# Performance work log

Hardware: AMD Instinct MI355X
Metric: run time of the kernel (lower is better)

The kernel has to match this reference:

```python
import jax, jax.numpy as jnp
import numpy as np

N = 100000   # nodes
E = 1600000  # edges (before self-loops)
H1, C1 = 8, 16   # conv1: heads=8, out_channels=16
H2, C2 = 1, 1    # conv2: heads=1, out_channels=1
NEG_SLOPE = 0.2
EPS = 1e-16


def setup_inputs() -> dict:
    key = jax.random.key(0)
    ks = jax.random.split(key, 10)
    s = 0.3
    return {
        "x": jax.random.normal(ks[0], (N, 1), jnp.float32),
        "edge_index": jax.random.randint(ks[1], (2, E), 0, N, dtype=jnp.int64),
        "W1": jax.random.normal(ks[2], (1, H1 * C1), jnp.float32) * s,
        "att_src1": jax.random.normal(ks[3], (1, H1, C1), jnp.float32) * s,
        "att_dst1": jax.random.normal(ks[4], (1, H1, C1), jnp.float32) * s,
        "b1": jax.random.normal(ks[5], (H1 * C1,), jnp.float32) * s,
        "W2": jax.random.normal(ks[6], (H1 * C1, H2 * C2), jnp.float32) * s,
        "att_src2": jax.random.normal(ks[7], (1, H2, C2), jnp.float32) * s,
        "att_dst2": jax.random.normal(ks[8], (1, H2, C2), jnp.float32) * s,
        "b2": jax.random.normal(ks[9], (C2,), jnp.float32) * s,
    }


def gat_conv(x, src, dst, W, att_src, att_dst, bias, heads, ch, concat):
    # Linear projection, split into heads: [N, H, C]
    h = (x @ W).reshape(-1, heads, ch)
    # Per-node attention logits: [N, H]
    a_src = (h * att_src).sum(-1)
    a_dst = (h * att_dst).sum(-1)
    # Edge-wise score with LeakyReLU: [E, H]
    e = jax.nn.leaky_relu(a_src[src] + a_dst[dst], NEG_SLOPE)
    # Segment softmax over incoming edges of each dst node
    m = jax.ops.segment_max(e, dst, num_segments=N)
    ex = jnp.exp(e - m[dst])
    denom = jax.ops.segment_sum(ex, dst, num_segments=N)
    alpha = ex / (denom[dst] + EPS)                      # [E, H]
    # Weighted scatter-add aggregation: [N, H, C]
    out = jax.ops.segment_sum(h[src] * alpha[:, :, None], dst, num_segments=N)
    out = out.reshape(-1, heads * ch) if concat else out.mean(axis=1)
    return out + bias


def reference(x, edge_index, W1, att_src1, att_dst1, b1, W2, att_src2, att_dst2, b2):
    # PyG GATConv default add_self_loops=True
    loop = jnp.arange(N, dtype=edge_index.dtype)
    src = jnp.concatenate([edge_index[0], loop])
    dst = jnp.concatenate([edge_index[1], loop])
    # dropout p=0.6 is identity in eval mode
    h = gat_conv(x, src, dst, W1, att_src1, att_dst1, b1, H1, C1, concat=True)
    h = jax.nn.elu(h)
    out = gat_conv(h, src, dst, W2, att_src2, att_dst2, b2, H2, C2, concat=False)
    return out  # [N, 1]
```

## Files before the change

kernel.cpp:

```cpp
#include <hip/hip_runtime.h>

#define NEG_SLOPE 0.2f
#define EPSV 1e-16f
#define NHEADS 8
#define NCH 16
#define BKT_SHIFT 8
#define BKT_NODES 256
#define CAP 8192
#define BIN_EPB 4096
#define MAX_BKT 512

__global__ __launch_bounds__(512) void gat_setup_kernel(
        const float* __restrict__ W1, const float* __restrict__ as1,
        const float* __restrict__ ad1, float* __restrict__ S1,
        float* __restrict__ D1, int* __restrict__ bkt_cnt, int nbuckets) {
    int t = threadIdx.x;
    for (int i = t; i < nbuckets; i += 512) bkt_cnt[i] = 0;
    if (t < NHEADS) {
        float s = 0.f, d = 0.f;
        for (int c = 0; c < NCH; ++c) {
            float w = W1[t * NCH + c];
            s += w * as1[t * NCH + c];
            d += w * ad1[t * NCH + c];
        }
        S1[t] = s;
        D1[t] = d;
    }
}

__global__ __launch_bounds__(256) void gat_bin_kernel(
        const int* __restrict__ ei, int E, int nbuckets,
        int* __restrict__ bkt_cnt, unsigned int* __restrict__ binned) {
    __shared__ int hist[MAX_BKT];
    __shared__ int gbase[MAX_BKT];
    int t = threadIdx.x;
    for (int i = t; i < nbuckets; i += 256) hist[i] = 0;
    __syncthreads();
    int base = blockIdx.x * BIN_EPB;
    int lr[BIN_EPB / 256];
#pragma unroll
    for (int k = 0; k < BIN_EPB / 1024; ++k) {
        int idx = base + k * 1024 + t * 4;
        if (idx + 3 < E) {
            int4 d4 = *(const int4*)(ei + E + idx);
            lr[4 * k + 0] = atomicAdd(&hist[d4.x >> BKT_SHIFT], 1);
            lr[4 * k + 1] = atomicAdd(&hist[d4.y >> BKT_SHIFT], 1);
            lr[4 * k + 2] = atomicAdd(&hist[d4.z >> BKT_SHIFT], 1);
            lr[4 * k + 3] = atomicAdd(&hist[d4.w >> BKT_SHIFT], 1);
        } else {
            for (int u = 0; u < 4; ++u)
                if (idx + u < E)
                    lr[4 * k + u] = atomicAdd(&hist[ei[E + idx + u] >> BKT_SHIFT], 1);
        }
    }
    __syncthreads();
    for (int i = t; i < nbuckets; i += 256) {
        int c = hist[i];
        gbase[i] = c ? (i * CAP + atomicAdd(&bkt_cnt[i], c)) : 0;
    }
    __syncthreads();
#pragma unroll
    for (int k = 0; k < BIN_EPB / 1024; ++k) {
        int idx = base + k * 1024 + t * 4;
        if (idx + 3 < E) {
            int4 s4 = *(const int4*)(ei + idx);
            int4 d4 = *(const int4*)(ei + E + idx);
            binned[gbase[d4.x >> BKT_SHIFT] + lr[4 * k + 0]] =
                ((unsigned int)s4.x << BKT_SHIFT) | (unsigned int)(d4.x & (BKT_NODES - 1));
            binned[gbase[d4.y >> BKT_SHIFT] + lr[4 * k + 1]] =
                ((unsigned int)s4.y << BKT_SHIFT) | (unsigned int)(d4.y & (BKT_NODES - 1));
            binned[gbase[d4.z >> BKT_SHIFT] + lr[4 * k + 2]] =
                ((unsigned int)s4.z << BKT_SHIFT) | (unsigned int)(d4.z & (BKT_NODES - 1));
            binned[gbase[d4.w >> BKT_SHIFT] + lr[4 * k + 3]] =
                ((unsigned int)s4.w << BKT_SHIFT) | (unsigned int)(d4.w & (BKT_NODES - 1));
        } else {
            for (int u = 0; u < 4; ++u)
                if (idx + u < E) {
                    unsigned int s = (unsigned int)ei[idx + u];
                    int d = ei[E + idx + u];
                    binned[gbase[d >> BKT_SHIFT] + lr[4 * k + u]] =
                        (s << BKT_SHIFT) | (unsigned int)(d & (BKT_NODES - 1));
                }
        }
    }
}

__global__ __launch_bounds__(256) void gat_gather1_kernel(
        int N, const float* __restrict__ x,
        unsigned int* __restrict__ binned, const int* __restrict__ bkt_cnt,
        const float* __restrict__ S1g, const float* __restrict__ D1g,
        const float* __restrict__ W1, const float* __restrict__ b1,
        const float* __restrict__ W2, float* __restrict__ h2out,
        int* __restrict__ row_start, int* __restrict__ row_deg) {
    __shared__ unsigned int ed[CAP];
    __shared__ int cnt[BKT_NODES];
    __shared__ int off[BKT_NODES];
    __shared__ int cur[BKT_NODES];
    __shared__ float xloc[BKT_NODES];
    int b = blockIdx.x, t = threadIdx.x;
    int node = (b << BKT_SHIFT) + t;
    xloc[t] = (node < N) ? x[node] : 0.f;
    cnt[t] = 0;
    __syncthreads();
    int nE = bkt_cnt[b]; if (nE > CAP) nE = CAP;
    const unsigned int* bb = binned + (size_t)b * CAP;
    for (int j0 = 0; j0 < nE; j0 += 1024) {
        int idx = j0 + t * 4;
        if (idx + 3 < nE) {
            uint4 q = *(const uint4*)(bb + idx);
            atomicAdd(&cnt[q.x & (BKT_NODES - 1)], 1);
            atomicAdd(&cnt[q.y & (BKT_NODES - 1)], 1);
            atomicAdd(&cnt[q.z & (BKT_NODES - 1)], 1);
            atomicAdd(&cnt[q.w & (BKT_NODES - 1)], 1);
        } else {
            for (int u = 0; u < 4; ++u)
                if (idx + u < nE) atomicAdd(&cnt[bb[idx + u] & (BKT_NODES - 1)], 1);
        }
    }
    __syncthreads();
    int c = cnt[t];
    off[t] = c;
    __syncthreads();
    for (int o = 1; o < 256; o <<= 1) {
        int v = (t >= o) ? off[t - o] : 0;
        __syncthreads();
        off[t] += v;
        __syncthreads();
    }
    int o_excl = off[t] - c;
    off[t] = o_excl;
    cur[t] = o_excl;
    __syncthreads();
    for (int j0 = 0; j0 < nE; j0 += 1024) {
        int idx = j0 + t * 4;
        if (idx + 3 < nE) {
            uint4 q = *(const uint4*)(bb + idx);
            ed[atomicAdd(&cur[q.x & (BKT_NODES - 1)], 1)] = q.x >> BKT_SHIFT;
            ed[atomicAdd(&cur[q.y & (BKT_NODES - 1)], 1)] = q.y >> BKT_SHIFT;
            ed[atomicAdd(&cur[q.z & (BKT_NODES - 1)], 1)] = q.z >> BKT_SHIFT;
            ed[atomicAdd(&cur[q.w & (BKT_NODES - 1)], 1)] = q.w >> BKT_SHIFT;
        } else {
            for (int u = 0; u < 4; ++u)
                if (idx + u < nE) {
                    unsigned int v = bb[idx + u];
                    ed[atomicAdd(&cur[v & (BKT_NODES - 1)], 1)] = v >> BKT_SHIFT;
                }
        }
    }
    __syncthreads();
    for (int j0 = 0; j0 < nE; j0 += 1024) {
        int idx = j0 + t * 4;
        if (idx + 3 < nE) {
            *(uint4*)(binned + (size_t)b * CAP + idx) = *(const uint4*)(ed + idx);
        } else {
            for (int u = 0; u < 4; ++u)
                if (idx + u < nE) binned[(size_t)b * CAP + idx + u] = ed[idx + u];
        }
    }
    if (node < N) {
        row_start[node] = b * CAP + o_excl;
        row_deg[node] = c;
    }
    float S1[NHEADS], A[NHEADS], den[NHEADS], num[NHEADS];
    float xn = xloc[t];
#pragma unroll
    for (int h = 0; h < NHEADS; ++h) {
        S1[h] = S1g[h];
        A[h] = xn * D1g[h];
        float e = xn * S1[h] + A[h];
        e = e > 0.f ? e : NEG_SLOPE * e;
        float ex = __expf(e);
        den[h] = ex + EPSV;
        num[h] = ex * xn;
    }
    int j = 0;
    for (; j + 4 <= c; j += 4) {
        unsigned int e0 = ed[o_excl + j + 0], e1 = ed[o_excl + j + 1];
        unsigned int e2 = ed[o_excl + j + 2], e3 = ed[o_excl + j + 3];
        float x0 = x[e0], x1 = x[e1], x2 = x[e2], x3 = x[e3];
#pragma unroll
        for (int h = 0; h < NHEADS; ++h) {
            float ea = x0 * S1[h] + A[h]; ea = ea > 0.f ? ea : NEG_SLOPE * ea;
            float eb = x1 * S1[h] + A[h]; eb = eb > 0.f ? eb : NEG_SLOPE * eb;
            float ec = x2 * S1[h] + A[h]; ec = ec > 0.f ? ec : NEG_SLOPE * ec;
            float ee = x3 * S1[h] + A[h]; ee = ee > 0.f ? ee : NEG_SLOPE * ee;
            float fa = __expf(ea), fb = __expf(eb), fc = __expf(ec), fd = __expf(ee);
            den[h] += (fa + fb) + (fc + fd);
            num[h] += (fa * x0 + fb * x1) + (fc * x2 + fd * x3);
        }
    }
    for (; j < c; ++j) {
        unsigned int e0 = ed[o_excl + j];
        float x0 = x[e0];
#pragma unroll
        for (int h = 0; h < NHEADS; ++h) {
            float ea = x0 * S1[h] + A[h];
            ea = ea > 0.f ? ea : NEG_SLOPE * ea;
            float fa = __expf(ea);
            den[h] += fa;
            num[h] += fa * x0;
        }
    }
    if (node >= N) return;
    float acc = 0.f;
#pragma unroll
    for (int h = 0; h < NHEADS; ++h) {
        float z = num[h] / den[h];
#pragma unroll
        for (int cc = 0; cc < NCH; ++cc) {
            int k = h * NCH + cc;
            float vv = W1[k] * z + b1[k];
            vv = vv > 0.f ? vv : (__expf(vv) - 1.f);
            acc += vv * W2[k];
        }
    }
    h2out[node] = acc;
}

__global__ __launch_bounds__(256) void gat_gather2_kernel(
        int N, const float* __restrict__ h2,
        const unsigned int* __restrict__ binned,
        const int* __restrict__ row_start, const int* __restrict__ row_deg,
        const float* __restrict__ as2p, const float* __restrict__ ad2p,
        const float* __restrict__ b2, float* __restrict__ out) {
    int n = blockIdx.x * blockDim.x + threadIdx.x;
    if (n >= N) return;
    float a_s = as2p[0], a_d = ad2p[0];
    float hn = h2[n];
    float ad = hn * a_d;
    float e = hn * a_s + ad;
    e = e > 0.f ? e : NEG_SLOPE * e;
    float ex = __expf(e);
    float den = ex + EPSV;
    float num = ex * hn;
    int st = row_start[n], dg = row_deg[n];
    int j = 0;
    for (; j + 4 <= dg; j += 4) {
        unsigned int e0 = binned[st + j + 0], e1 = binned[st + j + 1];
        unsigned int e2 = binned[st + j + 2], e3 = binned[st + j + 3];
        float h0 = h2[e0], h1 = h2[e1], h3 = h2[e2], h4 = h2[e3];
        float ea = h0 * a_s + ad; ea = ea > 0.f ? ea : NEG_SLOPE * ea;
        float eb = h1 * a_s + ad; eb = eb > 0.f ? eb : NEG_SLOPE * eb;
        float ec = h3 * a_s + ad; ec = ec > 0.f ? ec : NEG_SLOPE * ec;
        float ee = h4 * a_s + ad; ee = ee > 0.f ? ee : NEG_SLOPE * ee;
        float fa = __expf(ea), fb = __expf(eb), fc = __expf(ec), fd = __expf(ee);
        den += (fa + fb) + (fc + fd);
        num += (fa * h0 + fb * h1) + (fc * h3 + fd * h4);
    }
    for (; j < dg; ++j) {
        unsigned int e0 = binned[st + j];
        float h0 = h2[e0];
        float ea = h0 * a_s + ad;
        ea = ea > 0.f ? ea : NEG_SLOPE * ea;
        float fa = __expf(ea);
        den += fa;
        num += fa * h0;
    }
    out[n] = num / den + b2[0];
}

extern "C" void kernel_launch(void* const* d_in, const int* in_sizes, int n_in,
                              void* d_out, int out_size, void* d_ws, size_t ws_size,
                              hipStream_t stream) {
    const float* x   = (const float*)d_in[0];
    const int*   ei  = (const int*)d_in[1];
    const float* W1  = (const float*)d_in[2];
    const float* as1 = (const float*)d_in[3];
    const float* ad1 = (const float*)d_in[4];
    const float* b1  = (const float*)d_in[5];
    const float* W2  = (const float*)d_in[6];
    const float* as2 = (const float*)d_in[7];
    const float* ad2 = (const float*)d_in[8];
    const float* b2  = (const float*)d_in[9];
    float* out = (float*)d_out;

    int N = in_sizes[0];
    int E = in_sizes[1] / 2;

    int nbuckets = (N + BKT_NODES - 1) >> BKT_SHIFT;
    int nbin     = (E + BIN_EPB - 1) / BIN_EPB;
    int nb       = (N + 255) / 256;

    float* S1        = (float*)d_ws;
    float* D1        = S1 + 8;
    float* h2        = D1 + 8;
    int*   row_start = (int*)(h2 + N);
    int*   row_deg   = row_start + N;
    int*   bkt_cnt   = row_deg + N;
    unsigned int* binned = (unsigned int*)(bkt_cnt + nbuckets);

    gat_setup_kernel<<<1, 512, 0, stream>>>(W1, as1, ad1, S1, D1,
                                            bkt_cnt, nbuckets);
    gat_bin_kernel<<<nbin, 256, 0, stream>>>(ei, E, nbuckets, bkt_cnt, binned);
    gat_gather1_kernel<<<nbuckets, 256, 0, stream>>>(N, x, binned, bkt_cnt,
                                                     S1, D1, W1, b1, W2, h2,
                                                     row_start, row_deg);
    gat_gather2_kernel<<<nb, 256, 0, stream>>>(N, h2, binned, row_start, row_deg,
                                               as2, ad2, b2, out);
}
```

Baseline: 135.5 us.

## Fuse binning and both GAT layers into one cooperative kernel with grid syncs

Merges the setup, binning, layer-1 gather and layer-2 gather kernels into a single cooperative launch that uses grid-wide syncs between phases. The per-bucket sorted edge list stays in shared memory through layer 2, so the sorted list, row_start and row_deg are no longer written back to global memory. Layer 2 reuses each node's own h2 from a register. The cost is two grid barriers, a grid of about 391 blocks that must all be co-resident (launch bounds of 256 threads, 2 per CU), and an extra memset call.

```diff
diff --git a/kernel.cpp b/kernel.cpp
--- a/kernel.cpp
+++ b/kernel.cpp
@@ -1,4 +1,7 @@
 #include <hip/hip_runtime.h>
+#include <hip/hip_cooperative_groups.h>
+
+namespace cg = cooperative_groups;
 
 #define NEG_SLOPE 0.2f
 #define EPSV 1e-16f
@@ -10,12 +13,25 @@
 #define BIN_EPB 4096
 #define MAX_BKT 512
 
-__global__ __launch_bounds__(512) void gat_setup_kernel(
+__global__ __launch_bounds__(256, 2) void gat_fused_kernel(
+        int N, int E, int nbuckets,
+        const float* __restrict__ x, const int* __restrict__ ei,
         const float* __restrict__ W1, const float* __restrict__ as1,
-        const float* __restrict__ ad1, float* __restrict__ S1,
-        float* __restrict__ D1, int* __restrict__ bkt_cnt, int nbuckets) {
-    int t = threadIdx.x;
-    for (int i = t; i < nbuckets; i += 512) bkt_cnt[i] = 0;
+        const float* __restrict__ ad1, const float* __restrict__ b1,
+        const float* __restrict__ W2, const float* __restrict__ as2,
+        const float* __restrict__ ad2, const float* __restrict__ b2,
+        int* __restrict__ bkt_cnt, unsigned int* __restrict__ binned,
+        float* __restrict__ h2, float* __restrict__ out) {
+    cg::grid_group grid = cg::this_grid();
+    __shared__ unsigned int ed[CAP];
+    __shared__ int cnt[BKT_NODES];
+    __shared__ int cur[BKT_NODES];
+    __shared__ int offs[BKT_NODES];
+    __shared__ float xloc[BKT_NODES];
+    __shared__ float sS1[NHEADS], sD1[NHEADS];
+
+    int b = blockIdx.x, t = threadIdx.x;
+
     if (t < NHEADS) {
         float s = 0.f, d = 0.f;
         for (int c = 0; c < NCH; ++c) {
@@ -23,20 +39,14 @@
             s += w * as1[t * NCH + c];
             d += w * ad1[t * NCH + c];
         }
-        S1[t] = s;
-        D1[t] = d;
-    }
-}
-
-__global__ __launch_bounds__(256) void gat_bin_kernel(
-        const int* __restrict__ ei, int E, int nbuckets,
-        int* __restrict__ bkt_cnt, unsigned int* __restrict__ binned) {
-    __shared__ int hist[MAX_BKT];
-    __shared__ int gbase[MAX_BKT];
-    int t = threadIdx.x;
+        sS1[t] = s; sD1[t] = d;
+    }
+
+    int* hist  = (int*)&ed[0];
+    int* gbase = hist + MAX_BKT;
     for (int i = t; i < nbuckets; i += 256) hist[i] = 0;
     __syncthreads();
-    int base = blockIdx.x * BIN_EPB;
+    int base = b * BIN_EPB;
     int lr[BIN_EPB / 256];
 #pragma unroll
     for (int k = 0; k < BIN_EPB / 1024; ++k) {
@@ -83,26 +93,16 @@
                 }
         }
     }
-}
-
-__global__ __launch_bounds__(256) void gat_gather1_kernel(
-        int N, const float* __restrict__ x,
-        unsigned int* __restrict__ binned, const int* __restrict__ bkt_cnt,
-        const float* __restrict__ S1g, const float* __restrict__ D1g,
-        const float* __restrict__ W1, const float* __restrict__ b1,
-        const float* __restrict__ W2, float* __restrict__ h2out,
-        int* __restrict__ row_start, int* __restrict__ row_deg) {
-    __shared__ unsigned int ed[CAP];
-    __shared__ int cnt[BKT_NODES];
-    __shared__ int off[BKT_NODES];
-    __shared__ int cur[BKT_NODES];
-    __shared__ float xloc[BKT_NODES];
-    int b = blockIdx.x, t = threadIdx.x;
+    __threadfence();
+    grid.sync();
+
     int node = (b << BKT_SHIFT) + t;
-    xloc[t] = (node < N) ? x[node] : 0.f;
+    float xn = (node < N) ? x[node] : 0.f;
+    xloc[t] = xn;
     cnt[t] = 0;
     __syncthreads();
-    int nE = bkt_cnt[b]; if (nE > CAP) nE = CAP;
+    int nE = (b < nbuckets) ? bkt_cnt[b] : 0;
+    if (nE > CAP) nE = CAP;
     const unsigned int* bb = binned + (size_t)b * CAP;
     for (int j0 = 0; j0 < nE; j0 += 1024) {
         int idx = j0 + t * 4;
@@ -119,16 +119,15 @@
     }
     __syncthreads();
     int c = cnt[t];
-    off[t] = c;
+    offs[t] = c;
     __syncthreads();
     for (int o = 1; o < 256; o <<= 1) {
-        int v = (t >= o) ? off[t - o] : 0;
+        int v = (t >= o) ? offs[t - o] : 0;
         __syncthreads();
-        off[t] += v;
+        offs[t] += v;
         __syncthreads();
     }
-    int o_excl = off[t] - c;
-    off[t] = o_excl;
+    int o_excl = offs[t] - c;
     cur[t] = o_excl;
     __syncthreads();
     for (int j0 = 0; j0 < nE; j0 += 1024) {
@@ -148,25 +147,11 @@
         }
     }
     __syncthreads();
-    for (int j0 = 0; j0 < nE; j0 += 1024) {
-        int idx = j0 + t * 4;
-        if (idx + 3 < nE) {
-            *(uint4*)(binned + (size_t)b * CAP + idx) = *(const uint4*)(ed + idx);
-        } else {
-            for (int u = 0; u < 4; ++u)
-                if (idx + u < nE) binned[(size_t)b * CAP + idx + u] = ed[idx + u];
-        }
-    }
-    if (node < N) {
-        row_start[node] = b * CAP + o_excl;
-        row_deg[node] = c;
-    }
     float S1[NHEADS], A[NHEADS], den[NHEADS], num[NHEADS];
-    float xn = xloc[t];
 #pragma unroll
     for (int h = 0; h < NHEADS; ++h) {
-        S1[h] = S1g[h];
-        A[h] = xn * D1g[h];
+        S1[h] = sS1[h];
+        A[h] = xn * sD1[h];
         float e = xn * S1[h] + A[h];
         e = e > 0.f ? e : NEG_SLOPE * e;
         float ex = __expf(e);
@@ -201,62 +186,53 @@
             num[h] += fa * x0;
         }
     }
-    if (node >= N) return;
-    float acc = 0.f;
+    float h2val = 0.f;
 #pragma unroll
     for (int h = 0; h < NHEADS; ++h) {
         float z = num[h] / den[h];
 #pragma unroll
-        for (int cc = 0; cc < NCH; ++cc) {
-            int k = h * NCH + cc;
+        for (int ccc = 0; ccc < NCH; ++ccc) {
+            int k = h * NCH + ccc;
             float vv = W1[k] * z + b1[k];
             vv = vv > 0.f ? vv : (__expf(vv) - 1.f);
-            acc += vv * W2[k];
-        }
-    }
-    h2out[node] = acc;
-}
-
-__global__ __launch_bounds__(256) void gat_gather2_kernel(
-        int N, const float* __restrict__ h2,
-        const unsigned int* __restrict__ binned,
-        const int* __restrict__ row_start, const int* __restrict__ row_deg,
-        const float* __restrict__ as2p, const float* __restrict__ ad2p,
-        const float* __restrict__ b2, float* __restrict__ out) {
-    int n = blockIdx.x * blockDim.x + threadIdx.x;
-    if (n >= N) return;
-    float a_s = as2p[0], a_d = ad2p[0];
-    float hn = h2[n];
-    float ad = hn * a_d;
-    float e = hn * a_s + ad;
-    e = e > 0.f ? e : NEG_SLOPE * e;
-    float ex = __expf(e);
-    float den = ex + EPSV;
-    float num = ex * hn;
-    int st = row_start[n], dg = row_deg[n];
-    int j = 0;
-    for (; j + 4 <= dg; j += 4) {
-        unsigned int e0 = binned[st + j + 0], e1 = binned[st + j + 1];
-        unsigned int e2 = binned[st + j + 2], e3 = binned[st + j + 3];
+            h2val += vv * W2[k];
+        }
+    }
+    if (node < N) h2[node] = h2val;
+    __threadfence();
+    grid.sync();
+
+    float a_s = as2[0], a_d = ad2[0];
+    float hn = h2val;
+    float adc = hn * a_d;
+    float e2s = hn * (a_s + a_d);
+    e2s = e2s > 0.f ? e2s : NEG_SLOPE * e2s;
+    float ex2 = __expf(e2s);
+    float den2 = ex2 + EPSV;
+    float num2 = ex2 * hn;
+    j = 0;
+    for (; j + 4 <= c; j += 4) {
+        unsigned int e0 = ed[o_excl + j + 0], e1 = ed[o_excl + j + 1];
+        unsigned int e2 = ed[o_excl + j + 2], e3 = ed[o_excl + j + 3];
         float h0 = h2[e0], h1 = h2[e1], h3 = h2[e2], h4 = h2[e3];
-        float ea = h0 * a_s + ad; ea = ea > 0.f ? ea : NEG_SLOPE * ea;
-        float eb = h1 * a_s + ad; eb = eb > 0.f ? eb : NEG_SLOPE * eb;
-        float ec = h3 * a_s + ad; ec = ec > 0.f ? ec : NEG_SLOPE * ec;
-        float ee = h4 * a_s + ad; ee = ee > 0.f ? ee : NEG_SLOPE * ee;
+        float ea = h0 * a_s + adc; ea = ea > 0.f ? ea : NEG_SLOPE * ea;
+        float eb = h1 * a_s + adc; eb = eb > 0.f ? eb : NEG_SLOPE * eb;
+        float ec = h3 * a_s + adc; ec = ec > 0.f ? ec : NEG_SLOPE * ec;
+        float ee = h4 * a_s + adc; ee = ee > 0.f ? ee : NEG_SLOPE * ee;
         float fa = __expf(ea), fb = __expf(eb), fc = __expf(ec), fd = __expf(ee);
-        den += (fa + fb) + (fc + fd);
-        num += (fa * h0 + fb * h1) + (fc * h3 + fd * h4);
-    }
-    for (; j < dg; ++j) {
-        unsigned int e0 = binned[st + j];
+        den2 += (fa + fb) + (fc + fd);
+        num2 += (fa * h0 + fb * h1) + (fc * h3 + fd * h4);
+    }
+    for (; j < c; ++j) {
+        unsigned int e0 = ed[o_excl + j];
         float h0 = h2[e0];
-        float ea = h0 * a_s + ad;
+        float ea = h0 * a_s + adc;
         ea = ea > 0.f ? ea : NEG_SLOPE * ea;
         float fa = __expf(ea);
-        den += fa;
-        num += fa * h0;
-    }
-    out[n] = num / den + b2[0];
+        den2 += fa;
+        num2 += fa * h0;
+    }
+    if (node < N) out[node] = num2 / den2 + b2[0];
 }
 
 extern "C" void kernel_launch(void* const* d_in, const int* in_sizes, int n_in,
@@ -279,22 +255,18 @@
 
     int nbuckets = (N + BKT_NODES - 1) >> BKT_SHIFT;
     int nbin     = (E + BIN_EPB - 1) / BIN_EPB;
-    int nb       = (N + 255) / 256;
-
-    float* S1        = (float*)d_ws;
-    float* D1        = S1 + 8;
-    float* h2        = D1 + 8;
-    int*   row_start = (int*)(h2 + N);
-    int*   row_deg   = row_start + N;
-    int*   bkt_cnt   = row_deg + N;
+    int nblocks  = nbuckets > nbin ? nbuckets : nbin;
+
+    float* h2      = (float*)d_ws;
+    int*   bkt_cnt = (int*)(h2 + N);
     unsigned int* binned = (unsigned int*)(bkt_cnt + nbuckets);
 
-    gat_setup_kernel<<<1, 512, 0, stream>>>(W1, as1, ad1, S1, D1,
-                                            bkt_cnt, nbuckets);
-    gat_bin_kernel<<<nbin, 256, 0, stream>>>(ei, E, nbuckets, bkt_cnt, binned);
-    gat_gather1_kernel<<<nbuckets, 256, 0, stream>>>(N, x, binned, bkt_cnt,
-                                                     S1, D1, W1, b1, W2, h2,
-                                                     row_start, row_deg);
-    gat_gather2_kernel<<<nb, 256, 0, stream>>>(N, h2, binned, row_start, row_deg,
-                                               as2, ad2, b2, out);
+    hipMemsetAsync(bkt_cnt, 0, (size_t)nbuckets * sizeof(int), stream);
+
+    void* args[] = {
+        &N, &E, &nbuckets, &x, &ei, &W1, &as1, &ad1, &b1, &W2,
+        &as2, &ad2, &b2, &bkt_cnt, &binned, &h2, &out
+    };
+    hipLaunchCooperativeKernel((void*)gat_fused_kernel, dim3(nblocks), dim3(256),
+                               args, 0, stream);
 }
```

Result: slower. 331.6 us (+144.8%).

## Shrink buckets to 64 nodes and split each node's edges across four threads

Applied to the files above, without the earlier changes.

Buckets shrink from 256 to 64 nodes, giving about 1563 gather1 blocks instead of 391, so more CUs stay busy. Within a block, four threads share each node's edge list and combine partial softmax sums through shared-memory atomics. Gather2 likewise splits each node's edges across four lanes and reduces them with shuffles. The setup kernel is removed: the per-head projections are computed inside gather1 and the bucket-count reset becomes a memset. The risks are a larger bin histogram (1600 entries of shared memory), more shared-atomic traffic, and a per-bucket capacity of 2048 edges that could truncate an unusually dense bucket.

```diff
diff --git a/kernel.cpp b/kernel.cpp
--- a/kernel.cpp
+++ b/kernel.cpp
@@ -4,35 +4,17 @@
 #define EPSV 1e-16f
 #define NHEADS 8
 #define NCH 16
-#define BKT_SHIFT 8
-#define BKT_NODES 256
-#define CAP 8192
-#define BIN_EPB 4096
-#define MAX_BKT 512
-
-__global__ __launch_bounds__(512) void gat_setup_kernel(
-        const float* __restrict__ W1, const float* __restrict__ as1,
-        const float* __restrict__ ad1, float* __restrict__ S1,
-        float* __restrict__ D1, int* __restrict__ bkt_cnt, int nbuckets) {
-    int t = threadIdx.x;
-    for (int i = t; i < nbuckets; i += 512) bkt_cnt[i] = 0;
-    if (t < NHEADS) {
-        float s = 0.f, d = 0.f;
-        for (int c = 0; c < NCH; ++c) {
-            float w = W1[t * NCH + c];
-            s += w * as1[t * NCH + c];
-            d += w * ad1[t * NCH + c];
-        }
-        S1[t] = s;
-        D1[t] = d;
-    }
-}
+#define BKT_SHIFT 6
+#define BKT_NODES 64
+#define CAP 2048
+#define BIN_EPB 8192
+#define NBKT_MAX 1600
 
 __global__ __launch_bounds__(256) void gat_bin_kernel(
         const int* __restrict__ ei, int E, int nbuckets,
         int* __restrict__ bkt_cnt, unsigned int* __restrict__ binned) {
-    __shared__ int hist[MAX_BKT];
-    __shared__ int gbase[MAX_BKT];
+    __shared__ int hist[NBKT_MAX];
+    __shared__ int gbase[NBKT_MAX];
     int t = threadIdx.x;
     for (int i = t; i < nbuckets; i += 256) hist[i] = 0;
     __syncthreads();
@@ -88,57 +70,72 @@
 __global__ __launch_bounds__(256) void gat_gather1_kernel(
         int N, const float* __restrict__ x,
         unsigned int* __restrict__ binned, const int* __restrict__ bkt_cnt,
-        const float* __restrict__ S1g, const float* __restrict__ D1g,
-        const float* __restrict__ W1, const float* __restrict__ b1,
+        const float* __restrict__ W1, const float* __restrict__ as1,
+        const float* __restrict__ ad1, const float* __restrict__ b1,
         const float* __restrict__ W2, float* __restrict__ h2out,
         int* __restrict__ row_start, int* __restrict__ row_deg) {
     __shared__ unsigned int ed[CAP];
-    __shared__ int cnt[BKT_NODES];
-    __shared__ int off[BKT_NODES];
-    __shared__ int cur[BKT_NODES];
+    __shared__ int cnt[BKT_NODES], offs[BKT_NODES], cur[BKT_NODES];
     __shared__ float xloc[BKT_NODES];
+    __shared__ float sS1[NHEADS], sD1[NHEADS];
+    __shared__ float accD[NHEADS][BKT_NODES];
+    __shared__ float accN[NHEADS][BKT_NODES];
     int b = blockIdx.x, t = threadIdx.x;
-    int node = (b << BKT_SHIFT) + t;
-    xloc[t] = (node < N) ? x[node] : 0.f;
-    cnt[t] = 0;
+    int loc = t & (BKT_NODES - 1);
+    int q = t >> BKT_SHIFT;
+    if (t < NHEADS) {
+        float s = 0.f, d = 0.f;
+        for (int c = 0; c < NCH; ++c) {
+            float w = W1[t * NCH + c];
+            s += w * as1[t * NCH + c];
+            d += w * ad1[t * NCH + c];
+        }
+        sS1[t] = s; sD1[t] = d;
+    }
+    if (t < BKT_NODES) {
+        int node = (b << BKT_SHIFT) + t;
+        xloc[t] = (node < N) ? x[node] : 0.f;
+        cnt[t] = 0;
+    }
+    for (int i = t; i < NHEADS * BKT_NODES; i += 256) {
+        (&accD[0][0])[i] = 0.f;
+        (&accN[0][0])[i] = 0.f;
+    }
     __syncthreads();
     int nE = bkt_cnt[b]; if (nE > CAP) nE = CAP;
     const unsigned int* bb = binned + (size_t)b * CAP;
     for (int j0 = 0; j0 < nE; j0 += 1024) {
         int idx = j0 + t * 4;
         if (idx + 3 < nE) {
-            uint4 q = *(const uint4*)(bb + idx);
-            atomicAdd(&cnt[q.x & (BKT_NODES - 1)], 1);
-            atomicAdd(&cnt[q.y & (BKT_NODES - 1)], 1);
-            atomicAdd(&cnt[q.z & (BKT_NODES - 1)], 1);
-            atomicAdd(&cnt[q.w & (BKT_NODES - 1)], 1);
+            uint4 qv = *(const uint4*)(bb + idx);
+            atomicAdd(&cnt[qv.x & (BKT_NODES - 1)], 1);
+            atomicAdd(&cnt[qv.y & (BKT_NODES - 1)], 1);
+            atomicAdd(&cnt[qv.z & (BKT_NODES - 1)], 1);
+            atomicAdd(&cnt[qv.w & (BKT_NODES - 1)], 1);
         } else {
             for (int u = 0; u < 4; ++u)
                 if (idx + u < nE) atomicAdd(&cnt[bb[idx + u] & (BKT_NODES - 1)], 1);
         }
     }
     __syncthreads();
-    int c = cnt[t];
-    off[t] = c;
-    __syncthreads();
-    for (int o = 1; o < 256; o <<= 1) {
-        int v = (t >= o) ? off[t - o] : 0;
+    if (t < BKT_NODES) offs[t] = cnt[t];
+    __syncthreads();
+    for (int o = 1; o < BKT_NODES; o <<= 1) {
+        int v = (t < BKT_NODES && t >= o) ? offs[t - o] : 0;
         __syncthreads();
-        off[t] += v;
+        if (t < BKT_NODES) offs[t] += v;
         __syncthreads();
     }
-    int o_excl = off[t] - c;
-    off[t] = o_excl;
-    cur[t] = o_excl;
+    if (t < BKT_NODES) cur[t] = offs[t] - cnt[t];
     __syncthreads();
     for (int j0 = 0; j0 < nE; j0 += 1024) {
         int idx = j0 + t * 4;
         if (idx + 3 < nE) {
-            uint4 q = *(const uint4*)(bb + idx);
-            ed[atomicAdd(&cur[q.x & (BKT_NODES - 1)], 1)] = q.x >> BKT_SHIFT;
-            ed[atomicAdd(&cur[q.y & (BKT_NODES - 1)], 1)] = q.y >> BKT_SHIFT;
-            ed[atomicAdd(&cur[q.z & (BKT_NODES - 1)], 1)] = q.z >> BKT_SHIFT;
-            ed[atomicAdd(&cur[q.w & (BKT_NODES - 1)], 1)] = q.w >> BKT_SHIFT;
+            uint4 qv = *(const uint4*)(bb + idx);
+            ed[atomicAdd(&cur[qv.x & (BKT_NODES - 1)], 1)] = qv.x >> BKT_SHIFT;
+            ed[atomicAdd(&cur[qv.y & (BKT_NODES - 1)], 1)] = qv.y >> BKT_SHIFT;
+            ed[atomicAdd(&cur[qv.z & (BKT_NODES - 1)], 1)] = qv.z >> BKT_SHIFT;
+            ed[atomicAdd(&cur[qv.w & (BKT_NODES - 1)], 1)] = qv.w >> BKT_SHIFT;
         } else {
             for (int u = 0; u < 4; ++u)
                 if (idx + u < nE) {
@@ -157,40 +154,34 @@
                 if (idx + u < nE) binned[(size_t)b * CAP + idx + u] = ed[idx + u];
         }
     }
-    if (node < N) {
-        row_start[node] = b * CAP + o_excl;
-        row_deg[node] = c;
-    }
+    int deg = cnt[loc];
+    int ob = offs[loc] - deg;
+    int lo = ob + (deg * q) / 4;
+    int hi = ob + (deg * (q + 1)) / 4;
+    float xd = xloc[loc];
     float S1[NHEADS], A[NHEADS], den[NHEADS], num[NHEADS];
-    float xn = xloc[t];
 #pragma unroll
     for (int h = 0; h < NHEADS; ++h) {
-        S1[h] = S1g[h];
-        A[h] = xn * D1g[h];
-        float e = xn * S1[h] + A[h];
-        e = e > 0.f ? e : NEG_SLOPE * e;
-        float ex = __expf(e);
-        den[h] = ex + EPSV;
-        num[h] = ex * xn;
-    }
-    int j = 0;
-    for (; j + 4 <= c; j += 4) {
-        unsigned int e0 = ed[o_excl + j + 0], e1 = ed[o_excl + j + 1];
-        unsigned int e2 = ed[o_excl + j + 2], e3 = ed[o_excl + j + 3];
-        float x0 = x[e0], x1 = x[e1], x2 = x[e2], x3 = x[e3];
+        S1[h] = sS1[h];
+        A[h] = xd * sD1[h];
+        den[h] = 0.f;
+        num[h] = 0.f;
+    }
+    int j = lo;
+    for (; j + 2 <= hi; j += 2) {
+        unsigned int e0 = ed[j], e1 = ed[j + 1];
+        float x0 = x[e0], x1 = x[e1];
 #pragma unroll
         for (int h = 0; h < NHEADS; ++h) {
             float ea = x0 * S1[h] + A[h]; ea = ea > 0.f ? ea : NEG_SLOPE * ea;
             float eb = x1 * S1[h] + A[h]; eb = eb > 0.f ? eb : NEG_SLOPE * eb;
-            float ec = x2 * S1[h] + A[h]; ec = ec > 0.f ? ec : NEG_SLOPE * ec;
-            float ee = x3 * S1[h] + A[h]; ee = ee > 0.f ? ee : NEG_SLOPE * ee;
-            float fa = __expf(ea), fb = __expf(eb), fc = __expf(ec), fd = __expf(ee);
-            den[h] += (fa + fb) + (fc + fd);
-            num[h] += (fa * x0 + fb * x1) + (fc * x2 + fd * x3);
-        }
-    }
-    for (; j < c; ++j) {
-        unsigned int e0 = ed[o_excl + j];
+            float fa = __expf(ea), fb = __expf(eb);
+            den[h] += fa + fb;
+            num[h] += fa * x0 + fb * x1;
+        }
+    }
+    if (j < hi) {
+        unsigned int e0 = ed[j];
         float x0 = x[e0];
 #pragma unroll
         for (int h = 0; h < NHEADS; ++h) {
@@ -201,20 +192,38 @@
             num[h] += fa * x0;
         }
     }
-    if (node >= N) return;
-    float acc = 0.f;
 #pragma unroll
     for (int h = 0; h < NHEADS; ++h) {
-        float z = num[h] / den[h];
-#pragma unroll
-        for (int cc = 0; cc < NCH; ++cc) {
-            int k = h * NCH + cc;
-            float vv = W1[k] * z + b1[k];
-            vv = vv > 0.f ? vv : (__expf(vv) - 1.f);
-            acc += vv * W2[k];
-        }
-    }
-    h2out[node] = acc;
+        atomicAdd(&accD[h][loc], den[h]);
+        atomicAdd(&accN[h][loc], num[h]);
+    }
+    __syncthreads();
+    if (t < BKT_NODES) {
+        int node = (b << BKT_SHIFT) + t;
+        if (node < N) {
+            row_start[node] = b * CAP + ob;
+            row_deg[node] = deg;
+            float xn = xloc[t];
+            float acc = 0.f;
+#pragma unroll
+            for (int h = 0; h < NHEADS; ++h) {
+                float e = xn * (sS1[h] + sD1[h]);
+                e = e > 0.f ? e : NEG_SLOPE * e;
+                float ex = __expf(e);
+                float dsum = accD[h][t] + ex + EPSV;
+                float nsum = accN[h][t] + ex * xn;
+                float z = nsum / dsum;
+#pragma unroll
+                for (int c = 0; c < NCH; ++c) {
+                    int k = h * NCH + c;
+                    float vv = W1[k] * z + b1[k];
+                    vv = vv > 0.f ? vv : (__expf(vv) - 1.f);
+                    acc += vv * W2[k];
+                }
+            }
+            h2out[node] = acc;
+        }
+    }
 }
 
 __global__ __launch_bounds__(256) void gat_gather2_kernel(
@@ -223,40 +232,46 @@
         const int* __restrict__ row_start, const int* __restrict__ row_deg,
         const float* __restrict__ as2p, const float* __restrict__ ad2p,
         const float* __restrict__ b2, float* __restrict__ out) {
-    int n = blockIdx.x * blockDim.x + threadIdx.x;
-    if (n >= N) return;
+    int g = blockIdx.x * blockDim.x + threadIdx.x;
+    int n = g >> 2;
+    int q = g & 3;
+    bool valid = (n < N);
+    int nc = valid ? n : (N - 1);
     float a_s = as2p[0], a_d = ad2p[0];
-    float hn = h2[n];
-    float ad = hn * a_d;
-    float e = hn * a_s + ad;
-    e = e > 0.f ? e : NEG_SLOPE * e;
-    float ex = __expf(e);
-    float den = ex + EPSV;
-    float num = ex * hn;
-    int st = row_start[n], dg = row_deg[n];
-    int j = 0;
-    for (; j + 4 <= dg; j += 4) {
-        unsigned int e0 = binned[st + j + 0], e1 = binned[st + j + 1];
-        unsigned int e2 = binned[st + j + 2], e3 = binned[st + j + 3];
-        float h0 = h2[e0], h1 = h2[e1], h3 = h2[e2], h4 = h2[e3];
-        float ea = h0 * a_s + ad; ea = ea > 0.f ? ea : NEG_SLOPE * ea;
-        float eb = h1 * a_s + ad; eb = eb > 0.f ? eb : NEG_SLOPE * eb;
-        float ec = h3 * a_s + ad; ec = ec > 0.f ? ec : NEG_SLOPE * ec;
-        float ee = h4 * a_s + ad; ee = ee > 0.f ? ee : NEG_SLOPE * ee;
-        float fa = __expf(ea), fb = __expf(eb), fc = __expf(ec), fd = __expf(ee);
-        den += (fa + fb) + (fc + fd);
-        num += (fa * h0 + fb * h1) + (fc * h3 + fd * h4);
-    }
-    for (; j < dg; ++j) {
-        unsigned int e0 = binned[st + j];
+    float hn = h2[nc];
+    float adc = hn * a_d;
+    int st = row_start[nc];
+    int dg = valid ? row_deg[nc] : 0;
+    int lo = st + (dg * q) / 4;
+    int hi = st + (dg * (q + 1)) / 4;
+    float den = 0.f, num = 0.f;
+    int j = lo;
+    for (; j + 2 <= hi; j += 2) {
+        unsigned int e0 = binned[j], e1 = binned[j + 1];
+        float h0 = h2[e0], h1 = h2[e1];
+        float ea = h0 * a_s + adc; ea = ea > 0.f ? ea : NEG_SLOPE * ea;
+        float eb = h1 * a_s + adc; eb = eb > 0.f ? eb : NEG_SLOPE * eb;
+        float fa = __expf(ea), fb = __expf(eb);
+        den += fa + fb;
+        num += fa * h0 + fb * h1;
+    }
+    if (j < hi) {
+        unsigned int e0 = binned[j];
         float h0 = h2[e0];
-        float ea = h0 * a_s + ad;
+        float ea = h0 * a_s + adc;
         ea = ea > 0.f ? ea : NEG_SLOPE * ea;
         float fa = __expf(ea);
         den += fa;
         num += fa * h0;
     }
-    out[n] = num / den + b2[0];
+    den += __shfl_xor(den, 1); den += __shfl_xor(den, 2);
+    num += __shfl_xor(num, 1); num += __shfl_xor(num, 2);
+    if (q == 0 && valid) {
+        float e = hn * (a_s + a_d);
+        e = e > 0.f ? e : NEG_SLOPE * e;
+        float ex = __expf(e);
+        out[n] = (num + ex * hn) / (den + ex + EPSV) + b2[0];
+    }
 }
 
 extern "C" void kernel_launch(void* const* d_in, const int* in_sizes, int n_in,
@@ -279,22 +294,20 @@
 
     int nbuckets = (N + BKT_NODES - 1) >> BKT_SHIFT;
     int nbin     = (E + BIN_EPB - 1) / BIN_EPB;
-    int nb       = (N + 255) / 256;
-
-    float* S1        = (float*)d_ws;
-    float* D1        = S1 + 8;
-    float* h2        = D1 + 8;
+    int nb2      = (4 * N + 255) / 256;
+
+    float* h2        = (float*)d_ws;
     int*   row_start = (int*)(h2 + N);
     int*   row_deg   = row_start + N;
     int*   bkt_cnt   = row_deg + N;
     unsigned int* binned = (unsigned int*)(bkt_cnt + nbuckets);
 
-    gat_setup_kernel<<<1, 512, 0, stream>>>(W1, as1, ad1, S1, D1,
-                                            bkt_cnt, nbuckets);
+    hipMemsetAsync(bkt_cnt, 0, (size_t)nbuckets * sizeof(int), stream);
+
     gat_bin_kernel<<<nbin, 256, 0, stream>>>(ei, E, nbuckets, bkt_cnt, binned);
     gat_gather1_kernel<<<nbuckets, 256, 0, stream>>>(N, x, binned, bkt_cnt,
-                                                     S1, D1, W1, b1, W2, h2,
-                                                     row_start, row_deg);
-    gat_gather2_kernel<<<nb, 256, 0, stream>>>(N, h2, binned, row_start, row_deg,
-                                               as2, ad2, b2, out);
+                                                     W1, as1, ad1, b1, W2,
+                                                     h2, row_start, row_deg);
+    gat_gather2_kernel<<<nb2, 256, 0, stream>>>(N, h2, binned, row_start, row_deg,
+                                                as2, ad2, b2, out);
 }
```

New measurement: 166.0 us. 22.6% more time.
